# Kernel tuning notes

Measured on AMD Instinct MI355X. Metric: run time of the kernel, lower is better.

Reference implementation:

```python
import jax, jax.numpy as jnp
import numpy as np

B, S, T, DIM, H, W, HEADS = 4, 16, 16, 512, 32, 32, 8


def setup_inputs() -> dict:
    key = jax.random.key(0)
    ks = jax.random.split(key, 6)
    q = jax.random.normal(ks[0], (B, S, DIM, H, W), dtype=jnp.float32)
    k = jax.random.normal(ks[1], (B, T, DIM, H, W), dtype=jnp.float32)
    v = jax.random.normal(ks[2], (B, T, DIM, H, W), dtype=jnp.float32)
    Wq = jax.random.normal(ks[3], (DIM, DIM), dtype=jnp.float32) * (DIM ** -0.5)
    Wk = jax.random.normal(ks[4], (DIM, DIM), dtype=jnp.float32) * (DIM ** -0.5)
    Wv = jax.random.normal(ks[5], (DIM, DIM), dtype=jnp.float32) * (DIM ** -0.5)
    return {"q": q, "k": k, "v": v, "Wq": Wq, "Wk": Wk, "Wv": Wv, "heads": HEADS}


def reference(q, k, v, Wq, Wk, Wv, heads):
    b, s, d, h, w = q.shape
    t = k.shape[1]
    dh = d // heads
    scale = dh ** -0.5
    # pooled Q/K: spatial mean then linear (nn.Linear: x @ W.T)
    qm = jnp.mean(q, axis=(-1, -2)) @ Wq.T            # [B,S,D]
    km = jnp.mean(k, axis=(-1, -2)) @ Wk.T            # [B,T,D]
    # per-pixel V: permute(0,-1,-2,1,2) -> [B,W,H,T,D], flatten W*H (W-major, as torch)
    vp = jnp.transpose(v, (0, 4, 3, 1, 2)).reshape(b, w * h, t, d) @ Wv.T  # [B,HW,T,D]
    qh = qm.reshape(b, s, heads, dh) * scale          # [B,S,h,dh]
    kh = km.reshape(b, t, heads, dh)                  # [B,T,h,dh]
    vh = vp.reshape(b, w * h, t, heads, dh)           # [B,HW,T,h,dh]
    attn = jax.nn.softmax(jnp.einsum('bshd,bthd->bhst', qh, kh), axis=-1)  # [B,h,S,T]
    out = jnp.einsum('bhst,bpthd->bpshd', attn, vh)   # [B,HW,S,h,dh]
    # torch: out [B,HW,h,S,dh].permute(0,3,2,4,1) -> [B,S,h,dh,HW] -> view(B,S,D,H,W)
    out = jnp.transpose(out, (0, 2, 3, 4, 1)).reshape(b, s, d, h, w)
    return out
```

## Files before the change

kernel.cpp:

```cpp
#include <hip/hip_runtime.h>


__device__ __forceinline__ unsigned short f2bf(float f) {
  union { float f; unsigned int u; } x; x.f = f;
  unsigned int r = x.u + 0x7fffu + ((x.u >> 16) & 1u);
  return (unsigned short)(r >> 16);
}

typedef __attribute__((ext_vector_type(8))) __bf16 bf16x8;
typedef __attribute__((ext_vector_type(4))) float f32x4;

__global__ __launch_bounds__(256) void k_means(const float* __restrict__ q,
                                               const float* __restrict__ k,
                                               float* __restrict__ qm,
                                               float* __restrict__ km) {
  int n = blockIdx.x;
  const float* src = (n < 8192) ? q : k;
  float* dst = (n < 8192) ? qm : km;
  int chan = (n & 8191) * 4 + (threadIdx.x >> 6);
  int lane = threadIdx.x & 63;
  const float4* p = (const float4*)(src + (size_t)chan * 1024);
  float s = 0.f;
#pragma unroll
  for (int i = 0; i < 4; ++i) {
    float4 f = p[i * 64 + lane];
    s += f.x + f.y + f.z + f.w;
  }
#pragma unroll
  for (int off = 32; off > 0; off >>= 1) s += __shfl_down(s, off);
  if (lane == 0) dst[chan] = s * (1.0f / 1024.0f);
}

__global__ __launch_bounds__(256) void k_trans(const float* __restrict__ v,
                                               unsigned short* __restrict__ vT) {
  int tid = threadIdx.x;
  int m0 = blockIdx.x * 64, c0 = blockIdx.y * 64, bt = blockIdx.z;
  __shared__ float ls[64 * 65];
  const float* src = v + (size_t)bt * 524288;
#pragma unroll
  for (int p = 0; p < 4; ++p) {
    int r = p * 16 + (tid >> 4);
    int mm4 = (tid & 15) * 4;
    float4 f = *(const float4*)&src[(size_t)(c0 + r) * 1024 + m0 + mm4];
    ls[r * 65 + mm4 + 0] = f.x;
    ls[r * 65 + mm4 + 1] = f.y;
    ls[r * 65 + mm4 + 2] = f.z;
    ls[r * 65 + mm4 + 3] = f.w;
  }
  __syncthreads();
  unsigned short* dst = vT + (size_t)bt * 524288;
#pragma unroll
  for (int p = 0; p < 2; ++p) {
    int mm = p * 32 + (tid >> 3);
    int cr8 = (tid & 7) * 8;
    unsigned int w[4];
#pragma unroll
    for (int e = 0; e < 4; ++e) {
      unsigned short lo = f2bf(ls[(cr8 + 2 * e + 0) * 65 + mm]);
      unsigned short hi = f2bf(ls[(cr8 + 2 * e + 1) * 65 + mm]);
      w[e] = (unsigned int)lo | ((unsigned int)hi << 16);
    }
    uint4 pk = {w[0], w[1], w[2], w[3]};
    *(uint4*)&dst[(size_t)(m0 + mm) * 512 + c0 + cr8] = pk;
  }
}

__global__ __launch_bounds__(256) void k_attn(const float* __restrict__ qm,
                                              const float* __restrict__ km,
                                              const float* __restrict__ Wq,
                                              const float* __restrict__ Wk,
                                              const float* __restrict__ Wv,
                                              unsigned short* __restrict__ Wv_bf,
                                              float* __restrict__ attn) {
  int tid = threadIdx.x;
  int b = blockIdx.x >> 3, h = blockIdx.x & 7;
  {
    const float4* s4 = (const float4*)Wv;
#pragma unroll
    for (int i = 0; i < 8; ++i) {
      int idx = blockIdx.x * 256 + tid + i * 8192;
      float4 f = s4[idx];
      ushort4 u;
      u.x = f2bf(f.x); u.y = f2bf(f.y); u.z = f2bf(f.z); u.w = f2bf(f.w);
      *(ushort4*)&Wv_bf[(size_t)idx * 4] = u;
    }
  }
  __shared__ float WS[64 * 65];
  __shared__ float xS[16 * 64];
  __shared__ float qhS[16 * 65];
  __shared__ float khS[16 * 65];
  __shared__ float lg[16 * 17];
  int j = tid & 63, so = tid >> 6;
  float acc[4];

  acc[0] = acc[1] = acc[2] = acc[3] = 0.f;
  for (int c0 = 0; c0 < 512; c0 += 64) {
    __syncthreads();
#pragma unroll
    for (int p = 0; p < 4; ++p) {
      int r = p * 16 + (tid >> 4);
      int c4 = (tid & 15) * 4;
      float4 f = *(const float4*)&Wq[(size_t)(h * 64 + r) * 512 + c0 + c4];
      WS[r * 65 + c4 + 0] = f.x; WS[r * 65 + c4 + 1] = f.y;
      WS[r * 65 + c4 + 2] = f.z; WS[r * 65 + c4 + 3] = f.w;
    }
    {
      int s = tid >> 4;
      int c4 = (tid & 15) * 4;
      float4 f = *(const float4*)&qm[(size_t)(b * 16 + s) * 512 + c0 + c4];
      xS[s * 64 + c4 + 0] = f.x; xS[s * 64 + c4 + 1] = f.y;
      xS[s * 64 + c4 + 2] = f.z; xS[s * 64 + c4 + 3] = f.w;
    }
    __syncthreads();
    for (int cc = 0; cc < 64; ++cc) {
      float wv = WS[j * 65 + cc];
#pragma unroll
      for (int o = 0; o < 4; ++o) acc[o] += xS[(o * 4 + so) * 64 + cc] * wv;
    }
  }
#pragma unroll
  for (int o = 0; o < 4; ++o) qhS[(o * 4 + so) * 65 + j] = acc[o] * 0.125f;

  acc[0] = acc[1] = acc[2] = acc[3] = 0.f;
  for (int c0 = 0; c0 < 512; c0 += 64) {
    __syncthreads();
#pragma unroll
    for (int p = 0; p < 4; ++p) {
      int r = p * 16 + (tid >> 4);
      int c4 = (tid & 15) * 4;
      float4 f = *(const float4*)&Wk[(size_t)(h * 64 + r) * 512 + c0 + c4];
      WS[r * 65 + c4 + 0] = f.x; WS[r * 65 + c4 + 1] = f.y;
      WS[r * 65 + c4 + 2] = f.z; WS[r * 65 + c4 + 3] = f.w;
    }
    {
      int s = tid >> 4;
      int c4 = (tid & 15) * 4;
      float4 f = *(const float4*)&km[(size_t)(b * 16 + s) * 512 + c0 + c4];
      xS[s * 64 + c4 + 0] = f.x; xS[s * 64 + c4 + 1] = f.y;
      xS[s * 64 + c4 + 2] = f.z; xS[s * 64 + c4 + 3] = f.w;
    }
    __syncthreads();
    for (int cc = 0; cc < 64; ++cc) {
      float wv = WS[j * 65 + cc];
#pragma unroll
      for (int o = 0; o < 4; ++o) acc[o] += xS[(o * 4 + so) * 64 + cc] * wv;
    }
  }
#pragma unroll
  for (int o = 0; o < 4; ++o) khS[(o * 4 + so) * 65 + j] = acc[o];
  __syncthreads();

  {
    int s = tid >> 4, t = tid & 15;
    float a = 0.f;
    for (int jj = 0; jj < 64; ++jj) a += qhS[s * 65 + jj] * khS[t * 65 + jj];
    lg[s * 17 + t] = a;
  }
  __syncthreads();
  if (tid < 16) {
    int s = tid;
    float mx = -1e30f;
#pragma unroll
    for (int t = 0; t < 16; ++t) mx = fmaxf(mx, lg[s * 17 + t]);
    float e[16], sum = 0.f;
#pragma unroll
    for (int t = 0; t < 16; ++t) { e[t] = __expf(lg[s * 17 + t] - mx); sum += e[t]; }
    float inv = 1.0f / sum;
#pragma unroll
    for (int t = 0; t < 16; ++t) attn[((b * 8 + h) * 16 + s) * 16 + t] = e[t] * inv;
  }
}

__global__ __launch_bounds__(256) void k_gemm(const unsigned short* __restrict__ Wv_bf,
                                              const unsigned short* __restrict__ vT,
                                              float* __restrict__ VP) {
  int tid = threadIdx.x;
  int bx = blockIdx.x, by = blockIdx.y, bz = blockIdx.z;
  __shared__ __align__(16) unsigned short As[128 * 32];
  __shared__ __align__(16) unsigned short Bs[128 * 32];
  const unsigned short* Ag = Wv_bf + (size_t)(by * 128) * 512;
  const unsigned short* Bg = vT + (size_t)bz * 524288 + (size_t)(bx * 128) * 512;
  int r = tid >> 2;
  int c8 = (tid & 3) * 8;
  int lane = tid & 63, wave = tid >> 6;
  int wd = wave >> 1, wm = wave & 1;
  int l15 = lane & 15, quad = lane >> 4;

  f32x4 acc[4][4];
#pragma unroll
  for (int i = 0; i < 4; ++i)
#pragma unroll
    for (int j = 0; j < 4; ++j) acc[i][j] = (f32x4){0.f, 0.f, 0.f, 0.f};

  for (int kk = 0; kk < 16; ++kk) {
    int c0 = kk * 32;
    if (kk) __syncthreads();
    __builtin_amdgcn_global_load_lds(
        (const __attribute__((address_space(1))) void*)(Ag + (size_t)r * 512 + c0 + c8),
        (__attribute__((address_space(3))) void*)&As[tid * 8], 16, 0, 0);
    __builtin_amdgcn_global_load_lds(
        (const __attribute__((address_space(1))) void*)(Ag + (size_t)(r + 64) * 512 + c0 + c8),
        (__attribute__((address_space(3))) void*)&As[2048 + tid * 8], 16, 0, 0);
    __builtin_amdgcn_global_load_lds(
        (const __attribute__((address_space(1))) void*)(Bg + (size_t)r * 512 + c0 + c8),
        (__attribute__((address_space(3))) void*)&Bs[tid * 8], 16, 0, 0);
    __builtin_amdgcn_global_load_lds(
        (const __attribute__((address_space(1))) void*)(Bg + (size_t)(r + 64) * 512 + c0 + c8),
        (__attribute__((address_space(3))) void*)&Bs[2048 + tid * 8], 16, 0, 0);
    __syncthreads();

    bf16x8 af[4], bfr[4];
#pragma unroll
    for (int i = 0; i < 4; ++i)
      af[i] = *(const bf16x8*)&As[(wd * 64 + i * 16 + l15) * 32 + quad * 8];
#pragma unroll
    for (int j = 0; j < 4; ++j)
      bfr[j] = *(const bf16x8*)&Bs[(wm * 64 + j * 16 + l15) * 32 + quad * 8];
#pragma unroll
    for (int i = 0; i < 4; ++i)
#pragma unroll
      for (int j = 0; j < 4; ++j)
        acc[i][j] = __builtin_amdgcn_mfma_f32_16x16x32_bf16(af[i], bfr[j], acc[i][j], 0, 0, 0);
  }

  float* outp = VP + (size_t)bz * 524288;
#pragma unroll
  for (int i = 0; i < 4; ++i) {
#pragma unroll
    for (int j = 0; j < 4; ++j) {
      int m = bx * 128 + wm * 64 + j * 16 + l15;
#pragma unroll
      for (int rr = 0; rr < 4; ++rr) {
        int d = by * 128 + wd * 64 + i * 16 + quad * 4 + rr;
        outp[(size_t)d * 1024 + m] = acc[i][j][rr];
      }
    }
  }
}

__global__ __launch_bounds__(256) void k_mix(float* __restrict__ out,
                                             const float* __restrict__ attn) {
  int blk = blockIdx.x;
  int b = blk >> 9, d = blk & 511, h = d >> 6;
  int tid = threadIdx.x;
  __shared__ float VPs[16 * 1056];
  __shared__ float attnS[256];
  attnS[tid] = attn[(b * 8 + h) * 256 + tid];
  size_t base = ((size_t)(b * 16) * 512 + d) * 1024;
#pragma unroll
  for (int t = 0; t < 16; ++t) {
    float4 f = *(const float4*)&out[base + (size_t)t * 524288 + tid * 4];
    int m0 = tid * 4;
    int mi = t * 1056 + m0 + (m0 >> 5);
    VPs[mi + 0] = f.x; VPs[mi + 1] = f.y; VPs[mi + 2] = f.z; VPs[mi + 3] = f.w;
  }
  __syncthreads();

  float res[16][4];
#pragma unroll
  for (int j = 0; j < 4; ++j) {
    int p = tid * 4 + j;
    int m = ((p & 31) << 5) | (p >> 5);
    int mi = m + (m >> 5);
    float vp[16];
#pragma unroll
    for (int t = 0; t < 16; ++t) vp[t] = VPs[t * 1056 + mi];
#pragma unroll
    for (int s = 0; s < 16; ++s) {
      float a = 0.f;
#pragma unroll
      for (int t = 0; t < 16; ++t) a += attnS[s * 16 + t] * vp[t];
      res[s][j] = a;
    }
  }
#pragma unroll
  for (int s = 0; s < 16; ++s) {
    float4 f = {res[s][0], res[s][1], res[s][2], res[s][3]};
    *(float4*)&out[((size_t)(b * 16 + s) * 512 + d) * 1024 + tid * 4] = f;
  }
}

extern "C" void kernel_launch(void* const* d_in, const int* in_sizes, int n_in,
                              void* d_out, int out_size, void* d_ws, size_t ws_size,
                              hipStream_t stream) {
  const float* q  = (const float*)d_in[0];
  const float* k  = (const float*)d_in[1];
  const float* v  = (const float*)d_in[2];
  const float* Wq = (const float*)d_in[3];
  const float* Wk = (const float*)d_in[4];
  const float* Wv = (const float*)d_in[5];

  char* ws = (char*)d_ws;
  unsigned short* vT    = (unsigned short*)ws;
  unsigned short* Wv_bf = (unsigned short*)(ws + 67108864);
  float* qm   = (float*)(ws + 67633152);
  float* km   = (float*)(ws + 67764224);
  float* attn = (float*)(ws + 67895296);
  float* out  = (float*)d_out;

  k_means<<<16384, 256, 0, stream>>>(q, k, qm, km);
  k_trans<<<dim3(16, 8, 64), 256, 0, stream>>>(v, vT);
  k_attn<<<32, 256, 0, stream>>>(qm, km, Wq, Wk, Wv, Wv_bf, attn);
  k_gemm<<<dim3(8, 4, 64), 256, 0, stream>>>(Wv_bf, vT, out);
  k_mix<<<2048, 256, 0, stream>>>(out, attn);
}
```

Baseline: 562.3 us.

## Restructure attention-mix kernel into two T-chunks with per-wave S split

```diff
diff --git a/kernel.cpp b/kernel.cpp
--- a/kernel.cpp
+++ b/kernel.cpp
@@ -238,45 +238,62 @@
   }
 }
 
-__global__ __launch_bounds__(256) void k_mix(float* __restrict__ out,
-                                             const float* __restrict__ attn) {
+__global__ __launch_bounds__(256, 4) void k_mix(float* __restrict__ out,
+                                                const float* __restrict__ attn) {
   int blk = blockIdx.x;
   int b = blk >> 9, d = blk & 511, h = d >> 6;
   int tid = threadIdx.x;
-  __shared__ float VPs[16 * 1056];
+  __shared__ float VPs[8 * 1152];
   __shared__ float attnS[256];
   attnS[tid] = attn[(b * 8 + h) * 256 + tid];
+
+  int l = tid & 63, sg = tid >> 6;
+  int p0 = l * 16;
+  int phalf = 16 * (l & 1);
+  int pdiv = l >> 1;
+  int m0 = tid * 4;
+  int miw = m0 + 4 * (m0 >> 5);
+
   size_t base = ((size_t)(b * 16) * 512 + d) * 1024;
-#pragma unroll
-  for (int t = 0; t < 16; ++t) {
-    float4 f = *(const float4*)&out[base + (size_t)t * 524288 + tid * 4];
-    int m0 = tid * 4;
-    int mi = t * 1056 + m0 + (m0 >> 5);
-    VPs[mi + 0] = f.x; VPs[mi + 1] = f.y; VPs[mi + 2] = f.z; VPs[mi + 3] = f.w;
-  }
-  __syncthreads();
-
-  float res[16][4];
-#pragma unroll
-  for (int j = 0; j < 4; ++j) {
-    int p = tid * 4 + j;
-    int m = ((p & 31) << 5) | (p >> 5);
-    int mi = m + (m >> 5);
-    float vp[16];
-#pragma unroll
-    for (int t = 0; t < 16; ++t) vp[t] = VPs[t * 1056 + mi];
-#pragma unroll
-    for (int s = 0; s < 16; ++s) {
-      float a = 0.f;
-#pragma unroll
-      for (int t = 0; t < 16; ++t) a += attnS[s * 16 + t] * vp[t];
-      res[s][j] = a;
-    }
-  }
-#pragma unroll
-  for (int s = 0; s < 16; ++s) {
-    float4 f = {res[s][0], res[s][1], res[s][2], res[s][3]};
-    *(float4*)&out[((size_t)(b * 16 + s) * 512 + d) * 1024 + tid * 4] = f;
+  float res[4][16];
+#pragma unroll
+  for (int si = 0; si < 4; ++si)
+#pragma unroll
+    for (int u = 0; u < 16; ++u) res[si][u] = 0.f;
+
+  for (int ch = 0; ch < 2; ++ch) {
+    if (ch) __syncthreads();
+#pragma unroll
+    for (int t = 0; t < 8; ++t) {
+      float4 f = *(const float4*)&out[base + (size_t)(ch * 8 + t) * 524288 + m0];
+      *(float4*)&VPs[t * 1152 + miw] = f;
+    }
+    __syncthreads();
+#pragma unroll
+    for (int t = 0; t < 8; ++t) {
+      float a4[4];
+#pragma unroll
+      for (int si = 0; si < 4; ++si) a4[si] = attnS[(sg * 4 + si) * 16 + ch * 8 + t];
+      float vp[16];
+#pragma unroll
+      for (int u = 0; u < 16; ++u) vp[u] = VPs[t * 1152 + (phalf + u) * 36 + pdiv];
+#pragma unroll
+      for (int si = 0; si < 4; ++si)
+#pragma unroll
+        for (int u = 0; u < 16; ++u) res[si][u] += a4[si] * vp[u];
+    }
+  }
+
+#pragma unroll
+  for (int si = 0; si < 4; ++si) {
+    int s = sg * 4 + si;
+    float* op = &out[((size_t)(b * 16 + s) * 512 + d) * 1024 + p0];
+#pragma unroll
+    for (int e = 0; e < 4; ++e) {
+      float4 f = {res[si][e * 4 + 0], res[si][e * 4 + 1],
+                  res[si][e * 4 + 2], res[si][e * 4 + 3]};
+      *(float4*)&op[e * 4] = f;
+    }
   }
 }
 
```

After: 731.0 us. 1.3x slower.

## Fold pixel permutation into transpose kernel and drop LDS staging in mix

Applied to the files above, without the earlier changes.

```diff
diff --git a/kernel.cpp b/kernel.cpp
--- a/kernel.cpp
+++ b/kernel.cpp
@@ -61,7 +61,9 @@
       w[e] = (unsigned int)lo | ((unsigned int)hi << 16);
     }
     uint4 pk = {w[0], w[1], w[2], w[3]};
-    *(uint4*)&dst[(size_t)(m0 + mm) * 512 + c0 + cr8] = pk;
+    int x = m0 + mm;
+    int rr = ((x & 31) << 5) | (x >> 5);
+    *(uint4*)&dst[(size_t)rr * 512 + c0 + cr8] = pk;
   }
 }
 
@@ -71,7 +73,7 @@
                                               const float* __restrict__ Wk,
                                               const float* __restrict__ Wv,
                                               unsigned short* __restrict__ Wv_bf,
-                                              float* __restrict__ attn) {
+                                              float* __restrict__ attnT) {
   int tid = threadIdx.x;
   int b = blockIdx.x >> 3, h = blockIdx.x & 7;
   {
@@ -167,7 +169,8 @@
     for (int t = 0; t < 16; ++t) { e[t] = __expf(lg[s * 17 + t] - mx); sum += e[t]; }
     float inv = 1.0f / sum;
 #pragma unroll
-    for (int t = 0; t < 16; ++t) attn[((b * 8 + h) * 16 + s) * 16 + t] = e[t] * inv;
+    for (int t = 0; t < 16; ++t)
+      attnT[(blockIdx.x) * 256 + t * 16 + s] = e[t] * inv;
   }
 }
 
@@ -239,44 +242,34 @@
 }
 
 __global__ __launch_bounds__(256) void k_mix(float* __restrict__ out,
-                                             const float* __restrict__ attn) {
+                                             const float* __restrict__ attnT) {
   int blk = blockIdx.x;
   int b = blk >> 9, d = blk & 511, h = d >> 6;
   int tid = threadIdx.x;
-  __shared__ float VPs[16 * 1056];
-  __shared__ float attnS[256];
-  attnS[tid] = attn[(b * 8 + h) * 256 + tid];
-  size_t base = ((size_t)(b * 16) * 512 + d) * 1024;
+  const float* at = attnT + (b * 8 + h) * 256;
+  size_t base = ((size_t)(b * 16) * 512 + d) * 1024 + tid * 4;
+
+  float res[16][4];
+#pragma unroll
+  for (int s = 0; s < 16; ++s)
+#pragma unroll
+    for (int j = 0; j < 4; ++j) res[s][j] = 0.f;
+
 #pragma unroll
   for (int t = 0; t < 16; ++t) {
-    float4 f = *(const float4*)&out[base + (size_t)t * 524288 + tid * 4];
-    int m0 = tid * 4;
-    int mi = t * 1056 + m0 + (m0 >> 5);
-    VPs[mi + 0] = f.x; VPs[mi + 1] = f.y; VPs[mi + 2] = f.z; VPs[mi + 3] = f.w;
-  }
-  __syncthreads();
-
-  float res[16][4];
-#pragma unroll
-  for (int j = 0; j < 4; ++j) {
-    int p = tid * 4 + j;
-    int m = ((p & 31) << 5) | (p >> 5);
-    int mi = m + (m >> 5);
-    float vp[16];
-#pragma unroll
-    for (int t = 0; t < 16; ++t) vp[t] = VPs[t * 1056 + mi];
+    float4 vp = *(const float4*)&out[base + (size_t)t * 524288];
 #pragma unroll
     for (int s = 0; s < 16; ++s) {
-      float a = 0.f;
-#pragma unroll
-      for (int t = 0; t < 16; ++t) a += attnS[s * 16 + t] * vp[t];
-      res[s][j] = a;
-    }
-  }
+      float a = at[t * 16 + s];
+      res[s][0] += a * vp.x; res[s][1] += a * vp.y;
+      res[s][2] += a * vp.z; res[s][3] += a * vp.w;
+    }
+  }
+
 #pragma unroll
   for (int s = 0; s < 16; ++s) {
     float4 f = {res[s][0], res[s][1], res[s][2], res[s][3]};
-    *(float4*)&out[((size_t)(b * 16 + s) * 512 + d) * 1024 + tid * 4] = f;
+    *(float4*)&out[base + (size_t)s * 524288] = f;
   }
 }
 
@@ -293,14 +286,14 @@
   char* ws = (char*)d_ws;
   unsigned short* vT    = (unsigned short*)ws;
   unsigned short* Wv_bf = (unsigned short*)(ws + 67108864);
-  float* qm   = (float*)(ws + 67633152);
-  float* km   = (float*)(ws + 67764224);
-  float* attn = (float*)(ws + 67895296);
-  float* out  = (float*)d_out;
+  float* qm    = (float*)(ws + 67633152);
+  float* km    = (float*)(ws + 67764224);
+  float* attnT = (float*)(ws + 67895296);
+  float* out   = (float*)d_out;
 
   k_means<<<16384, 256, 0, stream>>>(q, k, qm, km);
   k_trans<<<dim3(16, 8, 64), 256, 0, stream>>>(v, vT);
-  k_attn<<<32, 256, 0, stream>>>(qm, km, Wq, Wk, Wv, Wv_bf, attn);
+  k_attn<<<32, 256, 0, stream>>>(qm, km, Wq, Wk, Wv, Wv_bf, attnT);
   k_gemm<<<dim3(8, 4, 64), 256, 0, stream>>>(Wv_bf, vT, out);
-  k_mix<<<2048, 256, 0, stream>>>(out, attn);
-}
+  k_mix<<<2048, 256, 0, stream>>>(out, attnT);
+}
```

After: 534.0 us. 1.05x faster.
